# Performance work log

Measured on AMD Instinct MI355X. Metric: run time of the kernel, lower is better.

The kernel has to match this reference:

```python
import jax, jax.numpy as jnp
import numpy as np

N_NODES = 50000
N_EDGES = 800000
H = 4


def setup_inputs() -> dict:
    key = jax.random.key(0)
    ks = jax.random.split(key, 12)
    s = 0.05
    return {
        "x_feat": jax.random.normal(ks[0], (N_NODES, 128), jnp.float32),
        "W_fc": jax.random.normal(ks[1], (128, 256), jnp.float32) * s,
        "W1": jax.random.normal(ks[2], (256, 256), jnp.float32) * s,
        "al1": jax.random.normal(ks[3], (H, 64), jnp.float32) * s,
        "ar1": jax.random.normal(ks[4], (H, 64), jnp.float32) * s,
        "b1": jnp.zeros((256,), jnp.float32),
        "W2": jax.random.normal(ks[5], (256, 256), jnp.float32) * s,
        "al2": jax.random.normal(ks[6], (H, 64), jnp.float32) * s,
        "ar2": jax.random.normal(ks[7], (H, 64), jnp.float32) * s,
        "b2": jnp.zeros((256,), jnp.float32),
        "src": jax.random.randint(ks[8], (N_EDGES,), 0, N_NODES, jnp.int64 if jax.config.jax_enable_x64 else jnp.int32),
        "dst": jax.random.randint(ks[9], (N_EDGES,), 0, N_NODES, jnp.int64 if jax.config.jax_enable_x64 else jnp.int32),
    }


def _gat_layer(x, src, dst, W, attn_l, attn_r, bias, n_nodes):
    """DGL GATConv: project, per-edge leaky-relu scores, edge softmax by dst,
    weighted segment-sum, + bias, ELU. Returns [N, H, dh]."""
    h, dh = attn_l.shape
    feat = (x @ W).reshape(n_nodes, h, dh)            # [N,H,dh]
    el = jnp.einsum('nhd,hd->nh', feat, attn_l)        # [N,H]
    er = jnp.einsum('nhd,hd->nh', feat, attn_r)        # [N,H]
    e = jax.nn.leaky_relu(el[src] + er[dst], 0.2)      # [E,H]
    # numerically stable segment softmax over incoming edges of each dst
    m = jax.ops.segment_max(e, dst, num_segments=n_nodes)
    ex = jnp.exp(e - m[dst])
    z = jax.ops.segment_sum(ex, dst, num_segments=n_nodes)
    a = ex / z[dst]                                    # [E,H]
    msg = feat[src] * a[:, :, None]                    # [E,H,dh]
    out = jax.ops.segment_sum(msg, dst, num_segments=n_nodes)  # [N,H,dh]
    out = out + bias.reshape(h, dh)
    return jax.nn.elu(out)


def reference(x_feat, W_fc, W1, al1, ar1, b1, W2, al2, ar2, b2, src, dst):
    n = x_feat.shape[0]
    h = jnp.tanh(x_feat @ W_fc)                         # [N,256] (dropout = identity in eval)
    g1 = _gat_layer(h, src, dst, W1, al1, ar1, b1, n)   # [N,4,64]
    g1 = g1.reshape(n, -1)                              # [N,256]
    g2 = _gat_layer(g1, src, dst, W2, al2, ar2, b2, n)  # [N,4,64]
    return jnp.mean(g2, axis=-2)                        # mean over heads -> [N,64]
```

## Files before the change

kernel.cpp:

```cpp
#include <hip/hip_runtime.h>
#include <hip/hip_bf16.h>
#include <hip/hip_fp16.h>
#include <math.h>


typedef __attribute__((ext_vector_type(8))) short bf16x8;
typedef __attribute__((ext_vector_type(4))) float f32x4;

__device__ __forceinline__ void split2(float v, short& h, short& l) {
    __hip_bfloat16 bh = __float2bfloat16(v);
    float r = v - __bfloat162float(bh);
    __hip_bfloat16 bl = __float2bfloat16(r);
    h = *reinterpret_cast<short*>(&bh);
    l = *reinterpret_cast<short*>(&bl);
}

__device__ __forceinline__ float fast_tanh(float x) {
    x = fminf(fmaxf(x, -15.f), 15.f);
    float e = __expf(2.f * x);
    return (e - 1.f) * __builtin_amdgcn_rcpf(e + 1.f);
}

__device__ __forceinline__ float leaky02(float x) { return x > 0.f ? x : 0.2f * x; }

__device__ __forceinline__ float sel_head(float4 q, int h) {
    float lo = (h & 1) ? q.y : q.x;
    float hi = (h & 1) ? q.w : q.z;
    return (h & 2) ? hi : lo;
}

__global__ __launch_bounds__(256) void wsplit3_kernel(
        const float* __restrict__ W0, short* __restrict__ B0h, short* __restrict__ B0l,
        const float* __restrict__ W1, short* __restrict__ B1h, short* __restrict__ B1l,
        const float* __restrict__ W2, short* __restrict__ B2h, short* __restrict__ B2l) {
    int idx = blockIdx.x * 256 + threadIdx.x;
    const float* W;
    short *Bh, *Bl;
    int K, rel;
    if (idx < 128 * 256) {
        W = W0; Bh = B0h; Bl = B0l; K = 128; rel = idx;
    } else if (idx < 128 * 256 + 256 * 256) {
        W = W1; Bh = B1h; Bl = B1l; K = 256; rel = idx - 128 * 256;
    } else if (idx < 128 * 256 + 2 * 256 * 256) {
        W = W2; Bh = B2h; Bl = B2l; K = 256; rel = idx - 128 * 256 - 256 * 256;
    } else {
        return;
    }
    int k = rel >> 8, n = rel & 255;
    short h, l;
    split2(W[rel], h, l);
    Bh[n * K + k] = h;
    Bl[n * K + k] = l;
}

__global__ __launch_bounds__(256) void xsplit_kernel(const float* __restrict__ X,
                                                     short* __restrict__ Xh,
                                                     short* __restrict__ Xl, int total) {
    int idx = blockIdx.x * 256 + threadIdx.x;
    if (idx >= total) return;
    short h, l;
    split2(X[idx], h, l);
    Xh[idx] = h;
    Xl[idx] = l;
}

template<bool TANH, bool ELER, bool SPLIT_OUT>
__global__ __launch_bounds__(256, 2) void mfma_gemm_kernel(
        const short* __restrict__ Ah, const short* __restrict__ Al,
        const short* __restrict__ Bh, const short* __restrict__ Bl,
        short* __restrict__ Oh, short* __restrict__ Ol, __half* __restrict__ O16,
        int M, int K,
        const float* __restrict__ al, const float* __restrict__ ar,
        float* __restrict__ el, float* __restrict__ er) {
    __shared__ __align__(16) short As_h[128 * 32];
    __shared__ __align__(16) short As_l[128 * 32];
    __shared__ __align__(16) short Bs_h[128 * 32];
    __shared__ __align__(16) short Bs_l[128 * 32];

    const int tid = threadIdx.x;
    const int row0 = blockIdx.x * 128;
    const int col0 = blockIdx.y * 128;

    const int sr = tid >> 1;
    const int sc = (tid & 1) << 4;

    const int lane = tid & 63;
    const int lr = lane & 15;
    const int lg = lane >> 4;
    const int wid = tid >> 6;
    const int wm = wid >> 1;
    const int wn = wid & 1;

    f32x4 acc[4][4];
#pragma unroll
    for (int i = 0; i < 4; ++i)
#pragma unroll
        for (int j = 0; j < 4; ++j) acc[i][j] = (f32x4){0.f, 0.f, 0.f, 0.f};

    for (int k0 = 0; k0 < K; k0 += 32) {
        {
            const short* ap_h = &Ah[(size_t)(row0 + sr) * K + k0 + sc];
            const short* ap_l = &Al[(size_t)(row0 + sr) * K + k0 + sc];
            *reinterpret_cast<bf16x8*>(&As_h[sr * 32 + sc])     = *reinterpret_cast<const bf16x8*>(ap_h);
            *reinterpret_cast<bf16x8*>(&As_h[sr * 32 + sc + 8]) = *reinterpret_cast<const bf16x8*>(ap_h + 8);
            *reinterpret_cast<bf16x8*>(&As_l[sr * 32 + sc])     = *reinterpret_cast<const bf16x8*>(ap_l);
            *reinterpret_cast<bf16x8*>(&As_l[sr * 32 + sc + 8]) = *reinterpret_cast<const bf16x8*>(ap_l + 8);
        }
        {
            const short* bhp = &Bh[(size_t)(col0 + sr) * K + k0 + sc];
            const short* blp = &Bl[(size_t)(col0 + sr) * K + k0 + sc];
            *reinterpret_cast<bf16x8*>(&Bs_h[sr * 32 + sc])     = *reinterpret_cast<const bf16x8*>(bhp);
            *reinterpret_cast<bf16x8*>(&Bs_h[sr * 32 + sc + 8]) = *reinterpret_cast<const bf16x8*>(bhp + 8);
            *reinterpret_cast<bf16x8*>(&Bs_l[sr * 32 + sc])     = *reinterpret_cast<const bf16x8*>(blp);
            *reinterpret_cast<bf16x8*>(&Bs_l[sr * 32 + sc + 8]) = *reinterpret_cast<const bf16x8*>(blp + 8);
        }
        __syncthreads();

        bf16x8 ah[4], av[4], bh[4], bv[4];
#pragma unroll
        for (int t = 0; t < 4; ++t) {
            int arow = (wm * 64 + t * 16 + lr) * 32 + lg * 8;
            int brow = (wn * 64 + t * 16 + lr) * 32 + lg * 8;
            ah[t] = *reinterpret_cast<const bf16x8*>(&As_h[arow]);
            av[t] = *reinterpret_cast<const bf16x8*>(&As_l[arow]);
            bh[t] = *reinterpret_cast<const bf16x8*>(&Bs_h[brow]);
            bv[t] = *reinterpret_cast<const bf16x8*>(&Bs_l[brow]);
        }
#pragma unroll
        for (int mt = 0; mt < 4; ++mt)
#pragma unroll
            for (int nt = 0; nt < 4; ++nt) {
                acc[mt][nt] = __builtin_amdgcn_mfma_f32_16x16x32_bf16(ah[mt], bh[nt], acc[mt][nt], 0, 0, 0);
                acc[mt][nt] = __builtin_amdgcn_mfma_f32_16x16x32_bf16(ah[mt], bv[nt], acc[mt][nt], 0, 0, 0);
                acc[mt][nt] = __builtin_amdgcn_mfma_f32_16x16x32_bf16(av[mt], bh[nt], acc[mt][nt], 0, 0, 0);
            }
        __syncthreads();
    }

    const int head = blockIdx.y * 2 + wn;
    float alv[4], arv[4];
    if (ELER) {
#pragma unroll
        for (int nt = 0; nt < 4; ++nt) {
            alv[nt] = al[head * 64 + nt * 16 + lr];
            arv[nt] = ar[head * 64 + nt * 16 + lr];
        }
    }
#pragma unroll
    for (int mt = 0; mt < 4; ++mt) {
#pragma unroll
        for (int r = 0; r < 4; ++r) {
            int row = row0 + wm * 64 + mt * 16 + lg * 4 + r;
            bool valid = row < M;
            float sl = 0.f, sr_ = 0.f;
#pragma unroll
            for (int nt = 0; nt < 4; ++nt) {
                float v = acc[mt][nt][r];
                if (TANH) v = fast_tanh(v);
                if (valid) {
                    size_t ci = (size_t)row * 256 + col0 + wn * 64 + nt * 16 + lr;
                    if (SPLIT_OUT) {
                        short hh, ll;
                        split2(v, hh, ll);
                        Oh[ci] = hh;
                        Ol[ci] = ll;
                    } else {
                        O16[ci] = __float2half(v);
                    }
                }
                if (ELER) { sl = fmaf(v, alv[nt], sl); sr_ = fmaf(v, arv[nt], sr_); }
            }
            if (ELER) {
#pragma unroll
                for (int mask = 1; mask < 16; mask <<= 1) {
                    sl  += __shfl_xor(sl, mask, 16);
                    sr_ += __shfl_xor(sr_, mask, 16);
                }
                if (valid && lr == 0) {
                    el[row * 4 + head] = sl;
                    er[row * 4 + head] = sr_;
                }
            }
        }
    }
}

__global__ void count_deg_kernel(const int* __restrict__ dst, int* __restrict__ deg, int E) {
    int i = blockIdx.x * blockDim.x + threadIdx.x;
    if (i < E) atomicAdd(&deg[dst[i]], 1);
}

__global__ __launch_bounds__(1024) void scan_kernel(const int* __restrict__ deg,
                                                    int* __restrict__ offs,
                                                    int* __restrict__ cursor, int n) {
    __shared__ int wsum[16];
    const int tid = threadIdx.x, lane = tid & 63, wv = tid >> 6;
    int carry = 0;
    for (int base = 0; base < n; base += 4096) {
        int i = base + tid * 4;
        int v0 = 0, v1 = 0, v2 = 0, v3 = 0;
        if (i + 3 < n) {
            int4 q = *reinterpret_cast<const int4*>(&deg[i]);
            v0 = q.x; v1 = q.y; v2 = q.z; v3 = q.w;
        } else if (i < n) {
            v0 = deg[i];
            if (i + 1 < n) v1 = deg[i + 1];
            if (i + 2 < n) v2 = deg[i + 2];
        }
        int s = v0 + v1 + v2 + v3;
        int incl = s;
#pragma unroll
        for (int d = 1; d < 64; d <<= 1) {
            int t = __shfl_up(incl, d, 64);
            if (lane >= d) incl += t;
        }
        if (lane == 63) wsum[wv] = incl;
        __syncthreads();
        int woff = 0, tot = 0;
#pragma unroll
        for (int w2 = 0; w2 < 16; ++w2) {
            int x = wsum[w2];
            if (w2 < wv) woff += x;
            tot += x;
        }
        int excl = carry + woff + incl - s;
        if (i < n) {
            int p0 = excl, p1 = p0 + v0, p2 = p1 + v1, p3 = p2 + v2;
            offs[i] = p0; cursor[i] = p0;
            if (i + 1 < n) { offs[i + 1] = p1; cursor[i + 1] = p1; }
            if (i + 2 < n) { offs[i + 2] = p2; cursor[i + 2] = p2; }
            if (i + 3 < n) { offs[i + 3] = p3; cursor[i + 3] = p3; }
        }
        carry += tot;
        __syncthreads();
    }
    if (tid == 0) offs[n] = carry;
}

__global__ void fill_csr_kernel(const int* __restrict__ src, const int* __restrict__ dst,
                                int* __restrict__ cursor, int* __restrict__ srcs_sorted,
                                int* __restrict__ dsts_sorted, int E) {
    int i = blockIdx.x * blockDim.x + threadIdx.x;
    if (i < E) {
        int d = dst[i];
        int pos = atomicAdd(&cursor[d], 1);
        srcs_sorted[pos] = src[i];
        dsts_sorted[pos] = d;
    }
}

__global__ __launch_bounds__(256) void edge_w_kernel(const int* __restrict__ srcs,
                                                     const int* __restrict__ dsts,
                                                     const float* __restrict__ el,
                                                     const float* __restrict__ er,
                                                     float4* __restrict__ w, int E) {
    int i = blockIdx.x * 256 + threadIdx.x;
    if (i >= E) return;
    int s = srcs[i], d = dsts[i];
    const float4 a = *reinterpret_cast<const float4*>(&el[(size_t)s * 4]);
    const float4 b = *reinterpret_cast<const float4*>(&er[(size_t)d * 4]);
    float4 o;
    o.x = __expf(leaky02(a.x + b.x));
    o.y = __expf(leaky02(a.y + b.y));
    o.z = __expf(leaky02(a.z + b.z));
    o.w = __expf(leaky02(a.w + b.w));
    w[i] = o;
}

template<bool FINAL>
__global__ __launch_bounds__(256) void gat_agg_kernel(const __half* __restrict__ feat,
                                                      const float4* __restrict__ wq,
                                                      const int* __restrict__ srcs,
                                                      const int* __restrict__ offs,
                                                      const float* __restrict__ bias,
                                                      float* __restrict__ out,
                                                      short* __restrict__ Gh,
                                                      short* __restrict__ Gl, int N) {
    const int tid = threadIdx.x;
    const int w = tid >> 6, l = tid & 63;
    const int n = blockIdx.x * 4 + w;
    if (n >= N) return;
    const int h = l >> 4;
    const int begin = offs[n];
    const int deg = offs[n + 1] - begin;
    const __half* fbase = feat + (size_t)l * 4;
    const float4 zero4 = make_float4(0.f, 0.f, 0.f, 0.f);

    float4 acc = zero4;
    float z = 0.f;

    for (int j = 0; j < deg; j += 8) {
        const int rem = deg - j;
        const int nb = __builtin_amdgcn_readfirstlane(begin + j);
        const int s0 = srcs[nb + 0];
        const int s1 = (rem > 1) ? srcs[nb + 1] : 0;
        const int s2 = (rem > 2) ? srcs[nb + 2] : 0;
        const int s3 = (rem > 3) ? srcs[nb + 3] : 0;
        const int s4 = (rem > 4) ? srcs[nb + 4] : 0;
        const int s5 = (rem > 5) ? srcs[nb + 5] : 0;
        const int s6 = (rem > 6) ? srcs[nb + 6] : 0;
        const int s7 = (rem > 7) ? srcs[nb + 7] : 0;
        const float4 w0 = wq[nb + 0];
        const float4 w1 = (rem > 1) ? wq[nb + 1] : zero4;
        const float4 w2 = (rem > 2) ? wq[nb + 2] : zero4;
        const float4 w3 = (rem > 3) ? wq[nb + 3] : zero4;
        const float4 w4 = (rem > 4) ? wq[nb + 4] : zero4;
        const float4 w5 = (rem > 5) ? wq[nb + 5] : zero4;
        const float4 w6 = (rem > 6) ? wq[nb + 6] : zero4;
        const float4 w7 = (rem > 7) ? wq[nb + 7] : zero4;
        const uint2 u0 = *reinterpret_cast<const uint2*>(fbase + (size_t)s0 * 256);
        const uint2 u1 = *reinterpret_cast<const uint2*>(fbase + (size_t)s1 * 256);
        const uint2 u2 = *reinterpret_cast<const uint2*>(fbase + (size_t)s2 * 256);
        const uint2 u3 = *reinterpret_cast<const uint2*>(fbase + (size_t)s3 * 256);
        const uint2 u4 = *reinterpret_cast<const uint2*>(fbase + (size_t)s4 * 256);
        const uint2 u5 = *reinterpret_cast<const uint2*>(fbase + (size_t)s5 * 256);
        const uint2 u6 = *reinterpret_cast<const uint2*>(fbase + (size_t)s6 * 256);
        const uint2 u7 = *reinterpret_cast<const uint2*>(fbase + (size_t)s7 * 256);

        const float e0 = sel_head(w0, h);
        const float e1 = sel_head(w1, h);
        const float e2 = sel_head(w2, h);
        const float e3 = sel_head(w3, h);
        const float e4 = sel_head(w4, h);
        const float e5 = sel_head(w5, h);
        const float e6 = sel_head(w6, h);
        const float e7 = sel_head(w7, h);
        z += ((e0 + e1) + (e2 + e3)) + ((e4 + e5) + (e6 + e7));

        auto fma4 = [&](float e, uint2 u) {
            const __half2* hp = reinterpret_cast<const __half2*>(&u);
            float2 a = __half22float2(hp[0]);
            float2 b = __half22float2(hp[1]);
            acc.x = fmaf(e, a.x, acc.x); acc.y = fmaf(e, a.y, acc.y);
            acc.z = fmaf(e, b.x, acc.z); acc.w = fmaf(e, b.y, acc.w);
        };
        fma4(e0, u0); fma4(e1, u1); fma4(e2, u2); fma4(e3, u3);
        fma4(e4, u4); fma4(e5, u5); fma4(e6, u6); fma4(e7, u7);
    }

    const float rz = (z > 0.f) ? __builtin_amdgcn_rcpf(z) : 0.f;
    const float4 bv = *reinterpret_cast<const float4*>(&bias[l * 4]);
    float4 v;
    v.x = fmaf(acc.x, rz, bv.x);
    v.y = fmaf(acc.y, rz, bv.y);
    v.z = fmaf(acc.z, rz, bv.z);
    v.w = fmaf(acc.w, rz, bv.w);
    v.x = v.x > 0.f ? v.x : expm1f(v.x);
    v.y = v.y > 0.f ? v.y : expm1f(v.y);
    v.z = v.z > 0.f ? v.z : expm1f(v.z);
    v.w = v.w > 0.f ? v.w : expm1f(v.w);

    if (!FINAL) {
        short4 hh, ll;
        split2(v.x, hh.x, ll.x);
        split2(v.y, hh.y, ll.y);
        split2(v.z, hh.z, ll.z);
        split2(v.w, hh.w, ll.w);
        *reinterpret_cast<short4*>(&Gh[(size_t)n * 256 + l * 4]) = hh;
        *reinterpret_cast<short4*>(&Gl[(size_t)n * 256 + l * 4]) = ll;
    } else {
        v.x += __shfl_down(v.x, 32, 64); v.y += __shfl_down(v.y, 32, 64);
        v.z += __shfl_down(v.z, 32, 64); v.w += __shfl_down(v.w, 32, 64);
        v.x += __shfl_down(v.x, 16, 64); v.y += __shfl_down(v.y, 16, 64);
        v.z += __shfl_down(v.z, 16, 64); v.w += __shfl_down(v.w, 16, 64);
        if (l < 16) {
            float4 o;
            o.x = 0.25f * v.x; o.y = 0.25f * v.y; o.z = 0.25f * v.z; o.w = 0.25f * v.w;
            *reinterpret_cast<float4*>(&out[(size_t)n * 64 + l * 4]) = o;
        }
    }
}

extern "C" void kernel_launch(void* const* d_in, const int* in_sizes, int n_in,
                              void* d_out, int out_size, void* d_ws, size_t ws_size,
                              hipStream_t stream) {
    const float* x_feat = (const float*)d_in[0];
    const float* W_fc   = (const float*)d_in[1];
    const float* W1     = (const float*)d_in[2];
    const float* al1    = (const float*)d_in[3];
    const float* ar1    = (const float*)d_in[4];
    const float* b1     = (const float*)d_in[5];
    const float* W2     = (const float*)d_in[6];
    const float* al2    = (const float*)d_in[7];
    const float* ar2    = (const float*)d_in[8];
    const float* b2     = (const float*)d_in[9];
    const int*   src    = (const int*)d_in[10];
    const int*   dst    = (const int*)d_in[11];
    float* out = (float*)d_out;

    const int N = in_sizes[0] / 128;
    const int E = in_sizes[10];
    const int NB = (N + 127) / 128;
    const int M_pad = NB * 128;

    char* ws = (char*)d_ws;
    size_t off = 0;
    auto alloc = [&](size_t bytes) -> void* {
        off = (off + 255) & ~(size_t)255;
        void* p = ws + off;
        off += bytes;
        return p;
    };
    short* Xh   = (short*)alloc((size_t)M_pad * 128 * 2);
    short* Xl   = (short*)alloc((size_t)M_pad * 128 * 2);
    short* Hh   = (short*)alloc((size_t)M_pad * 256 * 2);
    short* Hl   = (short*)alloc((size_t)M_pad * 256 * 2);
    __half* f16 = (__half*)alloc((size_t)M_pad * 256 * 2);
    float* el   = (float*)alloc((size_t)N * 4 * 4);
    float* er   = (float*)alloc((size_t)N * 4 * 4);
    int* deg    = (int*)alloc((size_t)N * 4);
    int* offs   = (int*)alloc((size_t)(N + 4) * 4);
    int* cursor = (int*)alloc((size_t)N * 4);
    int* srcs_sorted = (int*)alloc((size_t)(E + 8) * 4);
    int* dsts_sorted = (int*)alloc((size_t)(E + 8) * 4);
    float4* wq  = (float4*)alloc((size_t)(E + 8) * 16);
    short* Bfc_h = (short*)alloc((size_t)256 * 128 * 2);
    short* Bfc_l = (short*)alloc((size_t)256 * 128 * 2);
    short* B1_h  = (short*)alloc((size_t)256 * 256 * 2);
    short* B1_l  = (short*)alloc((size_t)256 * 256 * 2);
    short* B2_h  = (short*)alloc((size_t)256 * 256 * 2);
    short* B2_l  = (short*)alloc((size_t)256 * 256 * 2);

    const int eb = (E + 255) / 256;
    dim3 ggrid(NB, 2);
    const int agrid = (N + 3) / 4;

    hipMemsetAsync(deg, 0, (size_t)N * 4, stream);
    count_deg_kernel<<<eb, 256, 0, stream>>>(dst, deg, E);
    scan_kernel<<<1, 1024, 0, stream>>>(deg, offs, cursor, N);
    fill_csr_kernel<<<eb, 256, 0, stream>>>(src, dst, cursor, srcs_sorted, dsts_sorted, E);

    wsplit3_kernel<<<(128 * 256 + 2 * 256 * 256 + 255) / 256, 256, 0, stream>>>(
        W_fc, Bfc_h, Bfc_l, W1, B1_h, B1_l, W2, B2_h, B2_l);
    xsplit_kernel<<<(N * 128 + 255) / 256, 256, 0, stream>>>(x_feat, Xh, Xl, N * 128);

    mfma_gemm_kernel<true, false, true><<<ggrid, 256, 0, stream>>>(
        Xh, Xl, Bfc_h, Bfc_l, Hh, Hl, nullptr, N, 128, nullptr, nullptr, nullptr, nullptr);
    mfma_gemm_kernel<false, true, false><<<ggrid, 256, 0, stream>>>(
        Hh, Hl, B1_h, B1_l, nullptr, nullptr, f16, N, 256, al1, ar1, el, er);
    edge_w_kernel<<<eb, 256, 0, stream>>>(srcs_sorted, dsts_sorted, el, er, wq, E);
    gat_agg_kernel<false><<<agrid, 256, 0, stream>>>(
        f16, wq, srcs_sorted, offs, b1, nullptr, Hh, Hl, N);
    mfma_gemm_kernel<false, true, false><<<ggrid, 256, 0, stream>>>(
        Hh, Hl, B2_h, B2_l, nullptr, nullptr, f16, N, 256, al2, ar2, el, er);
    edge_w_kernel<<<eb, 256, 0, stream>>>(srcs_sorted, dsts_sorted, el, er, wq, E);
    gat_agg_kernel<true><<<agrid, 256, 0, stream>>>(
        f16, wq, srcs_sorted, offs, b2, out, nullptr, nullptr, N);
}
```

Baseline: 473.0 us.

## Double-buffer MFMA GEMM tiles with direct global-to-LDS async loads

Result: no change. 475.5 us (+0.5%).

```diff
diff --git a/kernel.cpp b/kernel.cpp
--- a/kernel.cpp
+++ b/kernel.cpp
@@ -6,6 +6,13 @@
 
 typedef __attribute__((ext_vector_type(8))) short bf16x8;
 typedef __attribute__((ext_vector_type(4))) float f32x4;
+
+typedef const __attribute__((address_space(1))) char gas_char;
+typedef __attribute__((address_space(3))) char las_char;
+
+__device__ __forceinline__ void gload16(const void* g, void* l) {
+    __builtin_amdgcn_global_load_lds((gas_char*)g, (las_char*)l, 16, 0, 0);
+}
 
 __device__ __forceinline__ void split2(float v, short& h, short& l) {
     __hip_bfloat16 bh = __float2bfloat16(v);
@@ -64,25 +71,22 @@
     Xl[idx] = l;
 }
 
-template<bool TANH, bool ELER, bool SPLIT_OUT>
+template<int K, bool TANH, bool ELER, bool SPLIT_OUT>
 __global__ __launch_bounds__(256, 2) void mfma_gemm_kernel(
         const short* __restrict__ Ah, const short* __restrict__ Al,
         const short* __restrict__ Bh, const short* __restrict__ Bl,
         short* __restrict__ Oh, short* __restrict__ Ol, __half* __restrict__ O16,
-        int M, int K,
+        int M,
         const float* __restrict__ al, const float* __restrict__ ar,
         float* __restrict__ el, float* __restrict__ er) {
-    __shared__ __align__(16) short As_h[128 * 32];
-    __shared__ __align__(16) short As_l[128 * 32];
-    __shared__ __align__(16) short Bs_h[128 * 32];
-    __shared__ __align__(16) short Bs_l[128 * 32];
+    __shared__ __align__(16) short As_h[2][128 * 32];
+    __shared__ __align__(16) short As_l[2][128 * 32];
+    __shared__ __align__(16) short Bs_h[2][128 * 32];
+    __shared__ __align__(16) short Bs_l[2][128 * 32];
 
     const int tid = threadIdx.x;
     const int row0 = blockIdx.x * 128;
     const int col0 = blockIdx.y * 128;
-
-    const int sr = tid >> 1;
-    const int sc = (tid & 1) << 4;
 
     const int lane = tid & 63;
     const int lr = lane & 15;
@@ -91,40 +95,50 @@
     const int wm = wid >> 1;
     const int wn = wid & 1;
 
+    const int srow = wid * 32 + (lane >> 2);
+    const int scol = (lane & 3) * 8;
+    const size_t aoff1 = (size_t)(row0 + srow) * K + scol;
+    const size_t aoff2 = aoff1 + (size_t)16 * K;
+    const size_t boff1 = (size_t)(col0 + srow) * K + scol;
+    const size_t boff2 = boff1 + (size_t)16 * K;
+    const int lbase1 = (wid * 32) * 32;
+    const int lbase2 = (wid * 32 + 16) * 32;
+
+    auto stage = [&](int buf, int k0) {
+        gload16(Ah + aoff1 + k0, &As_h[buf][lbase1]);
+        gload16(Ah + aoff2 + k0, &As_h[buf][lbase2]);
+        gload16(Al + aoff1 + k0, &As_l[buf][lbase1]);
+        gload16(Al + aoff2 + k0, &As_l[buf][lbase2]);
+        gload16(Bh + boff1 + k0, &Bs_h[buf][lbase1]);
+        gload16(Bh + boff2 + k0, &Bs_h[buf][lbase2]);
+        gload16(Bl + boff1 + k0, &Bs_l[buf][lbase1]);
+        gload16(Bl + boff2 + k0, &Bs_l[buf][lbase2]);
+    };
+
     f32x4 acc[4][4];
 #pragma unroll
     for (int i = 0; i < 4; ++i)
 #pragma unroll
         for (int j = 0; j < 4; ++j) acc[i][j] = (f32x4){0.f, 0.f, 0.f, 0.f};
 
-    for (int k0 = 0; k0 < K; k0 += 32) {
-        {
-            const short* ap_h = &Ah[(size_t)(row0 + sr) * K + k0 + sc];
-            const short* ap_l = &Al[(size_t)(row0 + sr) * K + k0 + sc];
-            *reinterpret_cast<bf16x8*>(&As_h[sr * 32 + sc])     = *reinterpret_cast<const bf16x8*>(ap_h);
-            *reinterpret_cast<bf16x8*>(&As_h[sr * 32 + sc + 8]) = *reinterpret_cast<const bf16x8*>(ap_h + 8);
-            *reinterpret_cast<bf16x8*>(&As_l[sr * 32 + sc])     = *reinterpret_cast<const bf16x8*>(ap_l);
-            *reinterpret_cast<bf16x8*>(&As_l[sr * 32 + sc + 8]) = *reinterpret_cast<const bf16x8*>(ap_l + 8);
-        }
-        {
-            const short* bhp = &Bh[(size_t)(col0 + sr) * K + k0 + sc];
-            const short* blp = &Bl[(size_t)(col0 + sr) * K + k0 + sc];
-            *reinterpret_cast<bf16x8*>(&Bs_h[sr * 32 + sc])     = *reinterpret_cast<const bf16x8*>(bhp);
-            *reinterpret_cast<bf16x8*>(&Bs_h[sr * 32 + sc + 8]) = *reinterpret_cast<const bf16x8*>(bhp + 8);
-            *reinterpret_cast<bf16x8*>(&Bs_l[sr * 32 + sc])     = *reinterpret_cast<const bf16x8*>(blp);
-            *reinterpret_cast<bf16x8*>(&Bs_l[sr * 32 + sc + 8]) = *reinterpret_cast<const bf16x8*>(blp + 8);
-        }
-        __syncthreads();
+    constexpr int NT = K / 32;
+    stage(0, 0);
+    __syncthreads();
+
+    int cur = 0;
+#pragma unroll
+    for (int t = 0; t < NT; ++t) {
+        if (t + 1 < NT) stage(cur ^ 1, (t + 1) * 32);
 
         bf16x8 ah[4], av[4], bh[4], bv[4];
 #pragma unroll
-        for (int t = 0; t < 4; ++t) {
-            int arow = (wm * 64 + t * 16 + lr) * 32 + lg * 8;
-            int brow = (wn * 64 + t * 16 + lr) * 32 + lg * 8;
-            ah[t] = *reinterpret_cast<const bf16x8*>(&As_h[arow]);
-            av[t] = *reinterpret_cast<const bf16x8*>(&As_l[arow]);
-            bh[t] = *reinterpret_cast<const bf16x8*>(&Bs_h[brow]);
-            bv[t] = *reinterpret_cast<const bf16x8*>(&Bs_l[brow]);
+        for (int q = 0; q < 4; ++q) {
+            int arow = (wm * 64 + q * 16 + lr) * 32 + lg * 8;
+            int brow = (wn * 64 + q * 16 + lr) * 32 + lg * 8;
+            ah[q] = *reinterpret_cast<const bf16x8*>(&As_h[cur][arow]);
+            av[q] = *reinterpret_cast<const bf16x8*>(&As_l[cur][arow]);
+            bh[q] = *reinterpret_cast<const bf16x8*>(&Bs_h[cur][brow]);
+            bv[q] = *reinterpret_cast<const bf16x8*>(&Bs_l[cur][brow]);
         }
 #pragma unroll
         for (int mt = 0; mt < 4; ++mt)
@@ -135,6 +149,7 @@
                 acc[mt][nt] = __builtin_amdgcn_mfma_f32_16x16x32_bf16(av[mt], bh[nt], acc[mt][nt], 0, 0, 0);
             }
         __syncthreads();
+        cur ^= 1;
     }
 
     const int head = blockIdx.y * 2 + wn;
@@ -434,15 +449,15 @@
         W_fc, Bfc_h, Bfc_l, W1, B1_h, B1_l, W2, B2_h, B2_l);
     xsplit_kernel<<<(N * 128 + 255) / 256, 256, 0, stream>>>(x_feat, Xh, Xl, N * 128);
 
-    mfma_gemm_kernel<true, false, true><<<ggrid, 256, 0, stream>>>(
-        Xh, Xl, Bfc_h, Bfc_l, Hh, Hl, nullptr, N, 128, nullptr, nullptr, nullptr, nullptr);
-    mfma_gemm_kernel<false, true, false><<<ggrid, 256, 0, stream>>>(
-        Hh, Hl, B1_h, B1_l, nullptr, nullptr, f16, N, 256, al1, ar1, el, er);
+    mfma_gemm_kernel<128, true, false, true><<<ggrid, 256, 0, stream>>>(
+        Xh, Xl, Bfc_h, Bfc_l, Hh, Hl, nullptr, N, nullptr, nullptr, nullptr, nullptr);
+    mfma_gemm_kernel<256, false, true, false><<<ggrid, 256, 0, stream>>>(
+        Hh, Hl, B1_h, B1_l, nullptr, nullptr, f16, N, al1, ar1, el, er);
     edge_w_kernel<<<eb, 256, 0, stream>>>(srcs_sorted, dsts_sorted, el, er, wq, E);
     gat_agg_kernel<false><<<agrid, 256, 0, stream>>>(
         f16, wq, srcs_sorted, offs, b1, nullptr, Hh, Hl, N);
-    mfma_gemm_kernel<false, true, false><<<ggrid, 256, 0, stream>>>(
-        Hh, Hl, B2_h, B2_l, nullptr, nullptr, f16, N, 256, al2, ar2, el, er);
+    mfma_gemm_kernel<256, false, true, false><<<ggrid, 256, 0, stream>>>(
+        Hh, Hl, B2_h, B2_l, nullptr, nullptr, f16, N, al2, ar2, el, er);
     edge_w_kernel<<<eb, 256, 0, stream>>>(srcs_sorted, dsts_sorted, el, er, wq, E);
     gat_agg_kernel<true><<<agrid, 256, 0, stream>>>(
         f16, wq, srcs_sorted, offs, b2, out, nullptr, nullptr, N);
```
